# Performance work log

Measured on AMD Instinct MI355X. Metric: run time of the kernel, lower is better.

The kernel has to match this reference:

```python
import jax, jax.numpy as jnp
import numpy as np

N_NODES = 5000
N_EDGES = 80000
HIDDEN = 128
NUM_RBF = 64
MAX_Z = 128
CUTOFF_UPPER = 5.0
LN_EPS = 1e-5


def setup_inputs() -> dict:
    key = jax.random.key(0)
    ks = jax.random.split(key, 24)
    H, R = HIDDEN, NUM_RBF
    def lin(k, out_d, in_d):
        s = 1.0 / np.sqrt(in_d)
        return jax.random.uniform(k, (out_d, in_d), jnp.float32, -s, s)
    def bias(k, out_d, in_d):
        s = 1.0 / np.sqrt(in_d)
        return jax.random.uniform(k, (out_d,), jnp.float32, -s, s)
    v = jax.random.normal(ks[3], (N_EDGES, 3), jnp.float32)
    v = v / jnp.linalg.norm(v, axis=-1, keepdims=True)
    return {
        "z": jax.random.randint(ks[0], (N_NODES,), 0, MAX_Z),
        "edge_index": jax.random.randint(ks[1], (2, N_EDGES), 0, N_NODES),
        "edge_weight": jax.random.uniform(ks[2], (N_EDGES,), jnp.float32) * CUTOFF_UPPER * 0.9,
        "edge_vec_norm": v,
        "edge_attr": jax.random.normal(ks[4], (N_EDGES, R), jnp.float32),
        "emb": jax.random.normal(ks[5], (MAX_Z, H), jnp.float32),
        "W_emb2": lin(ks[6], H, 2 * H), "b_emb2": bias(ks[7], H, 2 * H),
        "Wd1": lin(ks[8], H, R), "bd1": bias(ks[9], H, R),
        "Wd2": lin(ks[10], H, R), "bd2": bias(ks[11], H, R),
        "Wd3": lin(ks[12], H, R), "bd3": bias(ks[13], H, R),
        "Wt1": lin(ks[14], H, H), "Wt2": lin(ks[15], H, H), "Wt3": lin(ks[16], H, H),
        "Ws1": lin(ks[17], 2 * H, H), "bs1": bias(ks[18], 2 * H, H),
        "Ws2": lin(ks[19], 3 * H, 2 * H), "bs2": bias(ks[20], 3 * H, 2 * H),
        "ln_g": jnp.ones((H,), jnp.float32),
        "ln_b": jnp.zeros((H,), jnp.float32),
    }


def _skew(v):
    # v: [E,3] -> [E,3,3] skew-symmetric
    z = jnp.zeros_like(v[:, 0])
    return jnp.stack(
        [z, -v[:, 2], v[:, 1], v[:, 2], z, -v[:, 0], -v[:, 1], v[:, 0], z], axis=1
    ).reshape(-1, 3, 3)


def _sym(v):
    # symmetric traceless part of outer product (outer product already symmetric)
    outer = v[:, :, None] * v[:, None, :]
    tr = jnp.trace(outer, axis1=-2, axis2=-1) / 3.0
    return outer - tr[:, None, None] * jnp.eye(3, dtype=v.dtype)


def reference(z, edge_index, edge_weight, edge_vec_norm, edge_attr,
              emb, W_emb2, b_emb2, Wd1, bd1, Wd2, bd2, Wd3, bd3,
              Wt1, Wt2, Wt3, Ws1, bs1, Ws2, bs2, ln_g, ln_b):
    N = z.shape[0]
    H = emb.shape[1]
    src, dst = edge_index[0], edge_index[1]

    # atomic number message Zij: [E,H]
    Z = emb[z]
    Zij = jnp.concatenate([Z[src], Z[dst]], axis=-1) @ W_emb2.T + b_emb2

    # cosine cutoff (cutoff_lower = 0)
    cut = 0.5 * (jnp.cos(edge_weight * (jnp.pi / CUTOFF_UPPER)) + 1.0)
    cut = cut * (edge_weight < CUTOFF_UPPER).astype(edge_weight.dtype)
    C = cut[:, None] * Zij  # [E,H]

    f1 = (edge_attr @ Wd1.T + bd1) * C  # [E,H]
    f2 = (edge_attr @ Wd2.T + bd2) * C
    f3 = (edge_attr @ Wd3.T + bd3) * C

    eye = jnp.eye(3, dtype=C.dtype)
    Iij = f1[:, :, None, None] * eye  # [E,H,3,3]
    Aij = f2[:, :, None, None] * _skew(edge_vec_norm)[:, None, :, :]
    Sij = f3[:, :, None, None] * _sym(edge_vec_norm)[:, None, :, :]

    I = jax.ops.segment_sum(Iij, src, num_segments=N)  # [N,H,3,3]
    A = jax.ops.segment_sum(Aij, src, num_segments=N)
    S = jax.ops.segment_sum(Sij, src, num_segments=N)

    # Frobenius norm per channel, LayerNorm, scalar MLP
    tn = ((I + A + S) ** 2).sum((-2, -1))  # [N,H]
    mu = tn.mean(-1, keepdims=True)
    var = tn.var(-1, keepdims=True)
    norm = (tn - mu) / jnp.sqrt(var + LN_EPS) * ln_g + ln_b
    norm = jax.nn.silu(norm @ Ws1.T + bs1)
    norm = jax.nn.silu(norm @ Ws2.T + bs2)
    norm = norm.reshape(N, H, 3)

    I = jnp.einsum('nhij,gh->ngij', I, Wt1) * norm[:, :, 0, None, None]
    A = jnp.einsum('nhij,gh->ngij', A, Wt2) * norm[:, :, 1, None, None]
    S = jnp.einsum('nhij,gh->ngij', S, Wt3) * norm[:, :, 2, None, None]
    return I + A + S
```

## Files before the change

### kernel.cpp

```cpp
#include <hip/hip_runtime.h>
#include <hip/hip_bf16.h>

#define NN   5000
#define NP   5008
#define NE   80000
#define HID  128
#define NRBF 64
#define PI_OVER_5 0.6283185307179586f
#define LN_EPS 1e-5f

typedef unsigned short bf16_t;
typedef __attribute__((ext_vector_type(8))) short short8;
typedef __attribute__((ext_vector_type(4))) float floatx4;

__device__ __forceinline__ bf16_t to_bf16(float x){
    union { float f; unsigned int u; } v; v.f = x;
    unsigned int r = v.u + 0x7fffu + ((v.u >> 16) & 1u);
    return (bf16_t)(r >> 16);
}
__device__ __forceinline__ float from_bf16(bf16_t h){
    union { unsigned int u; float f; } v; v.u = ((unsigned int)h) << 16;
    return v.f;
}
__device__ __forceinline__ uint4 pack8(const float* s){
    float4 a = *(const float4*)s;
    float4 b = *(const float4*)(s + 4);
    uint4 o;
    o.x = to_bf16(a.x) | ((unsigned)to_bf16(a.y) << 16);
    o.y = to_bf16(a.z) | ((unsigned)to_bf16(a.w) << 16);
    o.z = to_bf16(b.x) | ((unsigned)to_bf16(b.y) << 16);
    o.w = to_bf16(b.z) | ((unsigned)to_bf16(b.w) << 16);
    return o;
}

__global__ __launch_bounds__(128) void k_embtab(
    const float* __restrict__ W_emb2, const float* __restrict__ emb,
    float* __restrict__ embL, float* __restrict__ embR)
{
    int t = blockIdx.x;
    int h = threadIdx.x;
    const float* er = emb + t * HID;
    const float* wl = W_emb2 + (size_t)h * (2 * HID);
    float sl = 0.f, sr = 0.f;
    #pragma unroll 8
    for (int k = 0; k < HID; k++){
        float e = er[k];
        sl += wl[k] * e;
        sr += wl[HID + k] * e;
    }
    embL[t * HID + h] = sl;
    embR[t * HID + h] = sr;
}

__global__ __launch_bounds__(256) void k_prep_wts(
    const float* __restrict__ Wd1, const float* __restrict__ Wd2, const float* __restrict__ Wd3,
    const float* __restrict__ bd1, const float* __restrict__ bd2, const float* __restrict__ bd3,
    const float* __restrict__ Wt1, const float* __restrict__ Wt2, const float* __restrict__ Wt3,
    const float* __restrict__ Ws1, const float* __restrict__ Ws2,
    bf16_t* __restrict__ Wcat, bf16_t* __restrict__ Wtc,
    bf16_t* __restrict__ Ws1b, bf16_t* __restrict__ Ws2b, float* __restrict__ bdcat)
{
    int t = blockIdx.x * 256 + threadIdx.x;
    int i8 = t * 8;
    const float* src; bf16_t* dst;
    if (i8 < 24576){
        int j = i8; int tb = j >> 13; int r = j & 8191;
        src = ((tb == 0) ? Wd1 : (tb == 1) ? Wd2 : Wd3) + r; dst = Wcat + j;
    } else if (i8 < 24576 + 49152){
        int j = i8 - 24576; int tb = j >> 14; int r = j & 16383;
        src = ((tb == 0) ? Wt1 : (tb == 1) ? Wt2 : Wt3) + r; dst = Wtc + j;
    } else if (i8 < 24576 + 49152 + 32768){
        int j = i8 - 73728; src = Ws1 + j; dst = Ws1b + j;
    } else {
        int j = i8 - 106496; src = Ws2 + j; dst = Ws2b + j;
    }
    *(uint4*)dst = pack8(src);
    if (t < 384){
        int tb2 = t >> 7, ch2 = t & 127;
        const float* bsrc = (tb2 == 0) ? bd1 : ((tb2 == 1) ? bd2 : bd3);
        bdcat[t] = bsrc[ch2];
    }
}

__global__ void k_count(const int* __restrict__ ei, int* __restrict__ counts){
    int e = blockIdx.x * 256 + threadIdx.x;
    if (e < NE) atomicAdd(&counts[ei[e]], 1);
}

__global__ __launch_bounds__(1024) void k_scan(
    const int* __restrict__ counts, int* __restrict__ offsets, int* __restrict__ cursor)
{
    __shared__ int s[1024];
    const int t = threadIdx.x;
    const int CH = 5;
    int base = t * CH;
    int loc[CH];
    int lsum = 0;
    #pragma unroll
    for (int u = 0; u < CH; u++){
        int i = base + u;
        int v = (i < NN) ? counts[i] : 0;
        loc[u] = lsum;
        lsum += v;
    }
    s[t] = lsum;
    __syncthreads();
    for (int d = 1; d < 1024; d <<= 1){
        int v = (t >= d) ? s[t - d] : 0;
        __syncthreads();
        s[t] += v;
        __syncthreads();
    }
    int excl = s[t] - lsum;
    #pragma unroll
    for (int u = 0; u < CH; u++){
        int i = base + u;
        if (i < NN){ int o = excl + loc[u]; offsets[i] = o; cursor[i] = o; }
    }
    if (t == 1023) offsets[NN] = s[1023];
}

__global__ void k_fill(const int* __restrict__ ei, const int* __restrict__ z,
                       const float* __restrict__ ew, const float* __restrict__ evn,
                       int* __restrict__ cursor, int* __restrict__ elist,
                       float2* __restrict__ meta, float* __restrict__ evn_p){
    int e = blockIdx.x * 256 + threadIdx.x;
    if (e < NE){
        int sN = ei[e], dN = ei[NE + e];
        int p = atomicAdd(&cursor[sN], 1);
        elist[p] = e;
        float w = ew[e];
        float c = (w < 5.0f) ? 0.5f * (__cosf(w * PI_OVER_5) + 1.0f) : 0.0f;
        meta[p] = make_float2(c, __int_as_float(z[sN] | (z[dN] << 8)));
        evn_p[p*3+0] = evn[e*3+0];
        evn_p[p*3+1] = evn[e*3+1];
        evn_p[p*3+2] = evn[e*3+2];
    }
}

__global__ __launch_bounds__(256) void k_edge(
    const float* __restrict__ attr, const int* __restrict__ elist,
    const float2* __restrict__ meta,
    const bf16_t* __restrict__ Wcat, const float* __restrict__ bdcat,
    const float* __restrict__ embL, const float* __restrict__ embR,
    const float* __restrict__ b_emb2,
    bf16_t* __restrict__ f1, bf16_t* __restrict__ f2, bf16_t* __restrict__ f3)
{
    __shared__ __align__(16) bf16_t sB[64 * 72];
    __shared__ float sCut[64];
    __shared__ int   sZ[64];

    const int tid = threadIdx.x;
    const int p0  = blockIdx.x * 64;

    {
        int r = tid >> 2, qt = tid & 3;
        int e = elist[p0 + r];
        const float* ar = attr + (size_t)e * NRBF + qt * 16;
        uint4 o0 = pack8(ar);
        uint4 o1 = pack8(ar + 8);
        *(uint4*)&sB[r * 72 + qt * 16]     = o0;
        *(uint4*)&sB[r * 72 + qt * 16 + 8] = o1;
    }
    if (tid < 64){
        float2 m = meta[p0 + tid];
        sCut[tid] = m.x;
        sZ[tid]   = __float_as_int(m.y);
    }
    __syncthreads();

    const int wv = tid >> 6, lane = tid & 63;
    const int col = lane & 15, q = lane >> 4;

    floatx4 acc[6][4];
    #pragma unroll
    for (int mt = 0; mt < 6; mt++)
        #pragma unroll
        for (int nt = 0; nt < 4; nt++)
            acc[mt][nt] = (floatx4)(0.f);

    #pragma unroll
    for (int s = 0; s < 2; s++){
        short8 bf[4];
        #pragma unroll
        for (int nt = 0; nt < 4; nt++){
            int r = nt * 16 + col;
            bf[nt] = *(const short8*)&sB[r * 72 + s * 32 + q * 8];
        }
        short8 af[6];
        #pragma unroll
        for (int t = 0; t < 3; t++)
            #pragma unroll
            for (int c = 0; c < 2; c++){
                int m = t * 128 + wv * 32 + c * 16 + col;
                af[t * 2 + c] = *(const short8*)(Wcat + (size_t)m * NRBF + s * 32 + q * 8);
            }
        #pragma unroll
        for (int mt = 0; mt < 6; mt++)
            #pragma unroll
            for (int nt = 0; nt < 4; nt++)
                acc[mt][nt] = __builtin_amdgcn_mfma_f32_16x16x32_bf16(
                    af[mt], bf[nt], acc[mt][nt], 0, 0, 0);
    }

    floatx4 be[2], bd[3][2];
    #pragma unroll
    for (int c = 0; c < 2; c++){
        int ch4 = wv * 32 + c * 16 + q * 4;
        be[c] = *(const floatx4*)(b_emb2 + ch4);
        #pragma unroll
        for (int t = 0; t < 3; t++)
            bd[t][c] = *(const floatx4*)(bdcat + t * 128 + ch4);
    }
    bf16_t* const fs[3] = {f1, f2, f3};
    #pragma unroll
    for (int nt = 0; nt < 4; nt++){
        int e = nt * 16 + col;
        float cut = sCut[e];
        int zp = sZ[e];
        int zs = zp & 255, zd = zp >> 8;
        size_t orow = (size_t)(p0 + e) * HID;
        #pragma unroll
        for (int c = 0; c < 2; c++){
            int ch4 = wv * 32 + c * 16 + q * 4;
            floatx4 L = *(const floatx4*)(embL + zs * HID + ch4);
            floatx4 R = *(const floatx4*)(embR + zd * HID + ch4);
            floatx4 Cv = (L + R + be[c]) * cut;
            #pragma unroll
            for (int t = 0; t < 3; t++){
                floatx4 v = (acc[t * 2 + c][nt] + bd[t][c]) * Cv;
                uint2 pk;
                pk.x = to_bf16(v[0]) | ((unsigned)to_bf16(v[1]) << 16);
                pk.y = to_bf16(v[2]) | ((unsigned)to_bf16(v[3]) << 16);
                *(uint2*)(fs[t] + orow + ch4) = pk;
            }
        }
    }
}

__global__ __launch_bounds__(128) void k_gather(
    const int* __restrict__ offsets, const float* __restrict__ evn_p,
    const bf16_t* __restrict__ f1, const bf16_t* __restrict__ f2, const bf16_t* __restrict__ f3,
    const float* __restrict__ ln_g, const float* __restrict__ ln_b,
    bf16_t* __restrict__ acc, bf16_t* __restrict__ ln_out)
{
    const int n = blockIdx.x, h = threadIdx.x;
    const int s = offsets[n], e_end = offsets[n + 1];
    float c=0, ax=0, ay=0, az=0, sxx=0, syy=0, szz=0, sxy=0, sxz=0, syz=0;
    for (int idx = s; idx < e_end; idx++){
        float vx = evn_p[idx*3+0], vy = evn_p[idx*3+1], vz = evn_p[idx*3+2];
        float t3 = (vx*vx + vy*vy + vz*vz) * (1.f/3.f);
        float a = from_bf16(f1[(size_t)idx * HID + h]);
        float b = from_bf16(f2[(size_t)idx * HID + h]);
        float d = from_bf16(f3[(size_t)idx * HID + h]);
        c += a;
        ax += b * vx; ay += b * vy; az += b * vz;
        sxx += d * (vx*vx - t3); syy += d * (vy*vy - t3); szz += d * (vz*vz - t3);
        sxy += d * (vx*vy); sxz += d * (vx*vz); syz += d * (vy*vz);
    }
    const int PS = NP * HID;
    const int base = n * HID + h;
    acc[0*PS+base]=to_bf16(c);   acc[1*PS+base]=to_bf16(ax);
    acc[2*PS+base]=to_bf16(ay);  acc[3*PS+base]=to_bf16(az);
    acc[4*PS+base]=to_bf16(sxx); acc[5*PS+base]=to_bf16(syy);
    acc[6*PS+base]=to_bf16(szz); acc[7*PS+base]=to_bf16(sxy);
    acc[8*PS+base]=to_bf16(sxz); acc[9*PS+base]=to_bf16(syz);

    float tn = 3.f*c*c + 2.f*c*(sxx+syy+szz)
             + sxx*sxx + syy*syy + szz*szz
             + 2.f*(sxy*sxy + sxz*sxz + syz*syz)
             + 2.f*(ax*ax + ay*ay + az*az);

    __shared__ float r1[128], r2[128];
    r1[h] = tn; r2[h] = tn * tn;
    __syncthreads();
    for (int st = 64; st > 0; st >>= 1){
        if (h < st){ r1[h] += r1[h + st]; r2[h] += r2[h + st]; }
        __syncthreads();
    }
    float mu  = r1[0] * (1.f / HID);
    float var = r2[0] * (1.f / HID) - mu * mu;
    ln_out[base] = to_bf16((tn - mu) * rsqrtf(var + LN_EPS) * ln_g[h] + ln_b[h]);
}

__global__ __launch_bounds__(256) void k_node(
    const bf16_t* __restrict__ lnb, const bf16_t* __restrict__ accb,
    const bf16_t* __restrict__ Ws1b, const float* __restrict__ bs1,
    const bf16_t* __restrict__ Ws2b, const float* __restrict__ bs2,
    const bf16_t* __restrict__ Wtc,
    float* __restrict__ out)
{
    __shared__ __align__(16) bf16_t h1s[16 * 280];
    __shared__ float nrms[16 * 392];

    const int tid = threadIdx.x;
    const int wv = tid >> 6, lane = tid & 63;
    const int col = lane & 15, q = lane >> 4;
    const int n0 = blockIdx.x * 16;

    {
        short8 a1[4];
        #pragma unroll
        for (int k = 0; k < 4; k++)
            a1[k] = *(const short8*)(lnb + (size_t)(n0 + col) * HID + k * 32 + q * 8);
        floatx4 c1[4];
        #pragma unroll
        for (int nt = 0; nt < 4; nt++) c1[nt] = (floatx4)(0.f);
        #pragma unroll
        for (int nt = 0; nt < 4; nt++){
            int cg = wv * 64 + nt * 16 + col;
            #pragma unroll
            for (int k = 0; k < 4; k++){
                short8 b = *(const short8*)(Ws1b + (size_t)cg * HID + k * 32 + q * 8);
                c1[nt] = __builtin_amdgcn_mfma_f32_16x16x32_bf16(a1[k], b, c1[nt], 0, 0, 0);
            }
        }
        #pragma unroll
        for (int nt = 0; nt < 4; nt++){
            int cg = wv * 64 + nt * 16 + col;
            float bias = bs1[cg];
            #pragma unroll
            for (int r = 0; r < 4; r++){
                float v = c1[nt][r] + bias;
                v = v / (1.f + __expf(-v));
                h1s[(q * 4 + r) * 280 + cg] = to_bf16(v);
            }
        }
    }
    __syncthreads();

    {
        short8 a2[8];
        #pragma unroll
        for (int k = 0; k < 8; k++)
            a2[k] = *(const short8*)&h1s[col * 280 + k * 32 + q * 8];
        floatx4 c2[6];
        #pragma unroll
        for (int nt = 0; nt < 6; nt++) c2[nt] = (floatx4)(0.f);
        #pragma unroll
        for (int nt = 0; nt < 6; nt++){
            int cg = wv * 96 + nt * 16 + col;
            #pragma unroll
            for (int k = 0; k < 8; k++){
                short8 b = *(const short8*)(Ws2b + (size_t)cg * 256 + k * 32 + q * 8);
                c2[nt] = __builtin_amdgcn_mfma_f32_16x16x32_bf16(a2[k], b, c2[nt], 0, 0, 0);
            }
        }
        #pragma unroll
        for (int nt = 0; nt < 6; nt++){
            int cg = wv * 96 + nt * 16 + col;
            float bias = bs2[cg];
            #pragma unroll
            for (int r = 0; r < 4; r++){
                float v = c2[nt][r] + bias;
                v = v / (1.f + __expf(-v));
                nrms[(q * 4 + r) * 392 + cg] = v;
            }
        }
    }
    __syncthreads();

    floatx4 cm[10][2];
    #pragma unroll
    for (int p = 0; p < 10; p++){
        #pragma unroll
        for (int nt = 0; nt < 2; nt++) cm[p][nt] = (floatx4)(0.f);
    }
    #pragma unroll
    for (int p = 0; p < 10; p++){
        const bf16_t* ap = accb + (size_t)p * NP * HID + (size_t)(n0 + col) * HID;
        short8 a3[4];
        #pragma unroll
        for (int k = 0; k < 4; k++)
            a3[k] = *(const short8*)(ap + k * 32 + q * 8);
        int tb = (p == 0) ? 0 : ((p < 4) ? 1 : 2);
        #pragma unroll
        for (int nt = 0; nt < 2; nt++){
            int g = wv * 32 + nt * 16 + col;
            const bf16_t* wp = Wtc + tb * 16384 + (size_t)g * HID;
            #pragma unroll
            for (int k = 0; k < 4; k++){
                short8 b = *(const short8*)(wp + k * 32 + q * 8);
                cm[p][nt] = __builtin_amdgcn_mfma_f32_16x16x32_bf16(a3[k], b, cm[p][nt], 0, 0, 0);
            }
        }
    }
    #pragma unroll
    for (int nt = 0; nt < 2; nt++){
        int g = wv * 32 + nt * 16 + col;
        #pragma unroll
        for (int r = 0; r < 4; r++){
            int node = q * 4 + r;
            int n = n0 + node;
            if (n < NN){
                float n0f = nrms[node * 392 + g * 3 + 0];
                float n1f = nrms[node * 392 + g * 3 + 1];
                float n2f = nrms[node * 392 + g * 3 + 2];
                float c   = cm[0][nt][r];
                float ax  = cm[1][nt][r], ay = cm[2][nt][r], az = cm[3][nt][r];
                float sxx = cm[4][nt][r], syy= cm[5][nt][r], szz= cm[6][nt][r];
                float sxy = cm[7][nt][r], sxz= cm[8][nt][r], syz= cm[9][nt][r];
                float* o = out + ((size_t)n * HID + g) * 9;
                o[0] = n0f*c + n2f*sxx;   o[1] = n2f*sxy - n1f*az;  o[2] = n2f*sxz + n1f*ay;
                o[3] = n2f*sxy + n1f*az;  o[4] = n0f*c + n2f*syy;   o[5] = n2f*syz - n1f*ax;
                o[6] = n2f*sxz - n1f*ay;  o[7] = n2f*syz + n1f*ax;  o[8] = n0f*c + n2f*szz;
            }
        }
    }
}

extern "C" void kernel_launch(void* const* d_in, const int* in_sizes, int n_in,
                              void* d_out, int out_size, void* d_ws, size_t ws_size,
                              hipStream_t stream)
{
    (void)in_sizes; (void)n_in; (void)out_size; (void)ws_size;
    const int*   z      = (const int*)  d_in[0];
    const int*   ei     = (const int*)  d_in[1];
    const float* ew     = (const float*)d_in[2];
    const float* evn    = (const float*)d_in[3];
    const float* attr   = (const float*)d_in[4];
    const float* emb    = (const float*)d_in[5];
    const float* W_emb2 = (const float*)d_in[6];
    const float* b_emb2 = (const float*)d_in[7];
    const float* Wd1 = (const float*)d_in[8];  const float* bd1 = (const float*)d_in[9];
    const float* Wd2 = (const float*)d_in[10]; const float* bd2 = (const float*)d_in[11];
    const float* Wd3 = (const float*)d_in[12]; const float* bd3 = (const float*)d_in[13];
    const float* Wt1 = (const float*)d_in[14]; const float* Wt2 = (const float*)d_in[15];
    const float* Wt3 = (const float*)d_in[16];
    const float* Ws1 = (const float*)d_in[17]; const float* bs1 = (const float*)d_in[18];
    const float* Ws2 = (const float*)d_in[19]; const float* bs2 = (const float*)d_in[20];
    const float* ln_g = (const float*)d_in[21]; const float* ln_b = (const float*)d_in[22];
    float* out = (float*)d_out;

    char* ws = (char*)d_ws;
    size_t o = 0;
    auto take = [&](size_t b)->size_t{ size_t c = o; o += (b + 255) & ~(size_t)255; return c; };
    size_t f1_o  = take((size_t)NE * HID * 2);
    size_t f2_o  = take((size_t)NE * HID * 2);
    size_t f3_o  = take((size_t)NE * HID * 2);
    size_t acc_o = take((size_t)10 * NP * HID * 2);
    size_t ln_of = take((size_t)NP * HID * 2);
    size_t eL_o  = take((size_t)128 * HID * 4);
    size_t eR_o  = take((size_t)128 * HID * 4);
    size_t cnt_o = take((size_t)NN * 4);
    size_t off_o = take((size_t)(NN + 1) * 4);
    size_t cur_o = take((size_t)NN * 4);
    size_t el_o  = take((size_t)NE * 4);
    size_t met_o = take((size_t)NE * 8);
    size_t evp_o = take((size_t)NE * 12);
    size_t wc_o  = take((size_t)384 * 64 * 2);
    size_t wt_o  = take((size_t)3 * 128 * 128 * 2);
    size_t w1_o  = take((size_t)256 * 128 * 2);
    size_t w2_o  = take((size_t)384 * 256 * 2);
    size_t bdc_o = take((size_t)384 * 4);

    bf16_t* f1 = (bf16_t*)(ws + f1_o);
    bf16_t* f2 = (bf16_t*)(ws + f2_o);
    bf16_t* f3 = (bf16_t*)(ws + f3_o);
    bf16_t* accb = (bf16_t*)(ws + acc_o);
    bf16_t* lnb  = (bf16_t*)(ws + ln_of);
    float* embL = (float*)(ws + eL_o);
    float* embR = (float*)(ws + eR_o);
    int* counts = (int*)(ws + cnt_o);
    int* offs   = (int*)(ws + off_o);
    int* cursor = (int*)(ws + cur_o);
    int* elist  = (int*)(ws + el_o);
    float2* meta = (float2*)(ws + met_o);
    float* evn_p = (float*)(ws + evp_o);
    bf16_t* Wcat = (bf16_t*)(ws + wc_o);
    bf16_t* Wtc  = (bf16_t*)(ws + wt_o);
    bf16_t* Ws1b = (bf16_t*)(ws + w1_o);
    bf16_t* Ws2b = (bf16_t*)(ws + w2_o);
    float* bdcat = (float*)(ws + bdc_o);

    hipMemsetAsync(counts, 0, (size_t)NN * 4, stream);

    k_prep_wts<<<100, 256, 0, stream>>>(Wd1, Wd2, Wd3, bd1, bd2, bd3,
                                        Wt1, Wt2, Wt3, Ws1, Ws2,
                                        Wcat, Wtc, Ws1b, Ws2b, bdcat);
    k_embtab<<<128, 128, 0, stream>>>(W_emb2, emb, embL, embR);
    k_count <<<(NE + 255) / 256, 256, 0, stream>>>(ei, counts);
    k_scan  <<<1, 1024, 0, stream>>>(counts, offs, cursor);
    k_fill  <<<(NE + 255) / 256, 256, 0, stream>>>(ei, z, ew, evn, cursor, elist, meta, evn_p);
    k_edge  <<<NE / 64, 256, 0, stream>>>(attr, elist, meta, Wcat, bdcat,
                                          embL, embR, b_emb2, f1, f2, f3);
    k_gather<<<NN, 128, 0, stream>>>(offs, evn_p, f1, f2, f3, ln_g, ln_b, accb, lnb);
    k_node  <<<(NN + 15) / 16, 256, 0, stream>>>(lnb, accb, Ws1b, bs1, Ws2b, bs2, Wtc, out);
}
```

Baseline: 229.8 us.

## Fuse all stages into one persistent cooperative kernel with grid syncs

```diff
diff --git a/kernel.cpp b/kernel.cpp
--- a/kernel.cpp
+++ b/kernel.cpp
@@ -1,5 +1,8 @@
 #include <hip/hip_runtime.h>
 #include <hip/hip_bf16.h>
+#include <hip/hip_cooperative_groups.h>
+
+namespace cg = cooperative_groups;
 
 #define NN   5000
 #define NP   5008
@@ -33,379 +36,367 @@
     return o;
 }
 
-__global__ __launch_bounds__(128) void k_embtab(
-    const float* __restrict__ W_emb2, const float* __restrict__ emb,
-    float* __restrict__ embL, float* __restrict__ embR)
+struct KP {
+    const int *z, *ei;
+    const float *ew, *evn, *attr, *emb, *W_emb2, *b_emb2;
+    const float *Wd1, *bd1, *Wd2, *bd2, *Wd3, *bd3;
+    const float *Wt1, *Wt2, *Wt3, *Ws1, *bs1, *Ws2, *bs2, *ln_g, *ln_b;
+    bf16_t *Wcat, *Wtc, *Ws1b, *Ws2b;
+    float *bdcat, *embL, *embR;
+    int *counts, *offs, *cursor, *elist;
+    float2 *meta; float *evn_p;
+    bf16_t *f1, *f2, *f3, *accb, *lnb;
+    float *out;
+};
+
+struct ShEdge {
+    bf16_t sB[64 * 72];
+    float  sCut[64];
+    int    sZ[64];
+};
+struct ShScan { int s[256]; };
+struct ShGat  { float r1[4], r2[4]; };
+struct ShNode {
+    bf16_t h1s[16 * 280];
+    bf16_t nrms[16 * 392];
+};
+union ShAll { ShEdge edge; ShScan scan; ShGat gat; ShNode node; };
+
+__global__ __launch_bounds__(256, 2) void k_all(KP P)
 {
-    int t = blockIdx.x;
-    int h = threadIdx.x;
-    const float* er = emb + t * HID;
-    const float* wl = W_emb2 + (size_t)h * (2 * HID);
-    float sl = 0.f, sr = 0.f;
-    #pragma unroll 8
-    for (int k = 0; k < HID; k++){
-        float e = er[k];
-        sl += wl[k] * e;
-        sr += wl[HID + k] * e;
-    }
-    embL[t * HID + h] = sl;
-    embR[t * HID + h] = sr;
-}
-
-__global__ __launch_bounds__(256) void k_prep_wts(
-    const float* __restrict__ Wd1, const float* __restrict__ Wd2, const float* __restrict__ Wd3,
-    const float* __restrict__ bd1, const float* __restrict__ bd2, const float* __restrict__ bd3,
-    const float* __restrict__ Wt1, const float* __restrict__ Wt2, const float* __restrict__ Wt3,
-    const float* __restrict__ Ws1, const float* __restrict__ Ws2,
-    bf16_t* __restrict__ Wcat, bf16_t* __restrict__ Wtc,
-    bf16_t* __restrict__ Ws1b, bf16_t* __restrict__ Ws2b, float* __restrict__ bdcat)
-{
-    int t = blockIdx.x * 256 + threadIdx.x;
-    int i8 = t * 8;
-    const float* src; bf16_t* dst;
-    if (i8 < 24576){
-        int j = i8; int tb = j >> 13; int r = j & 8191;
-        src = ((tb == 0) ? Wd1 : (tb == 1) ? Wd2 : Wd3) + r; dst = Wcat + j;
-    } else if (i8 < 24576 + 49152){
-        int j = i8 - 24576; int tb = j >> 14; int r = j & 16383;
-        src = ((tb == 0) ? Wt1 : (tb == 1) ? Wt2 : Wt3) + r; dst = Wtc + j;
-    } else if (i8 < 24576 + 49152 + 32768){
-        int j = i8 - 73728; src = Ws1 + j; dst = Ws1b + j;
-    } else {
-        int j = i8 - 106496; src = Ws2 + j; dst = Ws2b + j;
-    }
-    *(uint4*)dst = pack8(src);
-    if (t < 384){
-        int tb2 = t >> 7, ch2 = t & 127;
-        const float* bsrc = (tb2 == 0) ? bd1 : ((tb2 == 1) ? bd2 : bd3);
-        bdcat[t] = bsrc[ch2];
-    }
-}
-
-__global__ void k_count(const int* __restrict__ ei, int* __restrict__ counts){
-    int e = blockIdx.x * 256 + threadIdx.x;
-    if (e < NE) atomicAdd(&counts[ei[e]], 1);
-}
-
-__global__ __launch_bounds__(1024) void k_scan(
-    const int* __restrict__ counts, int* __restrict__ offsets, int* __restrict__ cursor)
-{
-    __shared__ int s[1024];
-    const int t = threadIdx.x;
-    const int CH = 5;
-    int base = t * CH;
-    int loc[CH];
-    int lsum = 0;
-    #pragma unroll
-    for (int u = 0; u < CH; u++){
-        int i = base + u;
-        int v = (i < NN) ? counts[i] : 0;
-        loc[u] = lsum;
-        lsum += v;
-    }
-    s[t] = lsum;
-    __syncthreads();
-    for (int d = 1; d < 1024; d <<= 1){
-        int v = (t >= d) ? s[t - d] : 0;
-        __syncthreads();
-        s[t] += v;
-        __syncthreads();
-    }
-    int excl = s[t] - lsum;
-    #pragma unroll
-    for (int u = 0; u < CH; u++){
-        int i = base + u;
-        if (i < NN){ int o = excl + loc[u]; offsets[i] = o; cursor[i] = o; }
-    }
-    if (t == 1023) offsets[NN] = s[1023];
-}
-
-__global__ void k_fill(const int* __restrict__ ei, const int* __restrict__ z,
-                       const float* __restrict__ ew, const float* __restrict__ evn,
-                       int* __restrict__ cursor, int* __restrict__ elist,
-                       float2* __restrict__ meta, float* __restrict__ evn_p){
-    int e = blockIdx.x * 256 + threadIdx.x;
-    if (e < NE){
-        int sN = ei[e], dN = ei[NE + e];
-        int p = atomicAdd(&cursor[sN], 1);
-        elist[p] = e;
-        float w = ew[e];
-        float c = (w < 5.0f) ? 0.5f * (__cosf(w * PI_OVER_5) + 1.0f) : 0.0f;
-        meta[p] = make_float2(c, __int_as_float(z[sN] | (z[dN] << 8)));
-        evn_p[p*3+0] = evn[e*3+0];
-        evn_p[p*3+1] = evn[e*3+1];
-        evn_p[p*3+2] = evn[e*3+2];
-    }
-}
-
-__global__ __launch_bounds__(256) void k_edge(
-    const float* __restrict__ attr, const int* __restrict__ elist,
-    const float2* __restrict__ meta,
-    const bf16_t* __restrict__ Wcat, const float* __restrict__ bdcat,
-    const float* __restrict__ embL, const float* __restrict__ embR,
-    const float* __restrict__ b_emb2,
-    bf16_t* __restrict__ f1, bf16_t* __restrict__ f2, bf16_t* __restrict__ f3)
-{
-    __shared__ __align__(16) bf16_t sB[64 * 72];
-    __shared__ float sCut[64];
-    __shared__ int   sZ[64];
+    cg::grid_group grid = cg::this_grid();
+    __shared__ __align__(16) ShAll sh;
 
     const int tid = threadIdx.x;
-    const int p0  = blockIdx.x * 64;
-
-    {
-        int r = tid >> 2, qt = tid & 3;
-        int e = elist[p0 + r];
-        const float* ar = attr + (size_t)e * NRBF + qt * 16;
-        uint4 o0 = pack8(ar);
-        uint4 o1 = pack8(ar + 8);
-        *(uint4*)&sB[r * 72 + qt * 16]     = o0;
-        *(uint4*)&sB[r * 72 + qt * 16 + 8] = o1;
-    }
-    if (tid < 64){
-        float2 m = meta[p0 + tid];
-        sCut[tid] = m.x;
-        sZ[tid]   = __float_as_int(m.y);
-    }
-    __syncthreads();
-
+    const int bid = blockIdx.x;
+    const int nblk = gridDim.x;
+    const int gthreads = nblk * 256;
+    const int gt = bid * 256 + tid;
     const int wv = tid >> 6, lane = tid & 63;
     const int col = lane & 15, q = lane >> 4;
 
-    floatx4 acc[6][4];
-    #pragma unroll
-    for (int mt = 0; mt < 6; mt++)
-        #pragma unroll
-        for (int nt = 0; nt < 4; nt++)
-            acc[mt][nt] = (floatx4)(0.f);
-
-    #pragma unroll
-    for (int s = 0; s < 2; s++){
-        short8 bf[4];
-        #pragma unroll
-        for (int nt = 0; nt < 4; nt++){
-            int r = nt * 16 + col;
-            bf[nt] = *(const short8*)&sB[r * 72 + s * 32 + q * 8];
-        }
-        short8 af[6];
-        #pragma unroll
-        for (int t = 0; t < 3; t++)
-            #pragma unroll
-            for (int c = 0; c < 2; c++){
-                int m = t * 128 + wv * 32 + c * 16 + col;
-                af[t * 2 + c] = *(const short8*)(Wcat + (size_t)m * NRBF + s * 32 + q * 8);
-            }
+    for (int t = gt; t < 25600; t += gthreads){
+        int i8 = t * 8;
+        const float* src; bf16_t* dst;
+        if (i8 < 24576){
+            int j = i8; int tb = j >> 13; int r = j & 8191;
+            src = ((tb == 0) ? P.Wd1 : (tb == 1) ? P.Wd2 : P.Wd3) + r; dst = P.Wcat + j;
+        } else if (i8 < 24576 + 49152){
+            int j = i8 - 24576; int tb = j >> 14; int r = j & 16383;
+            src = ((tb == 0) ? P.Wt1 : (tb == 1) ? P.Wt2 : P.Wt3) + r; dst = P.Wtc + j;
+        } else if (i8 < 24576 + 49152 + 32768){
+            int j = i8 - 73728; src = P.Ws1 + j; dst = P.Ws1b + j;
+        } else {
+            int j = i8 - 106496; src = P.Ws2 + j; dst = P.Ws2b + j;
+        }
+        *(uint4*)dst = pack8(src);
+        if (t < 384){
+            int tb2 = t >> 7, ch2 = t & 127;
+            const float* bsrc = (tb2 == 0) ? P.bd1 : ((tb2 == 1) ? P.bd2 : P.bd3);
+            P.bdcat[t] = bsrc[ch2];
+        }
+    }
+    for (int t = gt; t < 32768; t += gthreads){
+        int type = t >> 8; int rest = t & 255;
+        int half = rest >> 7; int h = rest & 127;
+        const float* wl = P.W_emb2 + (size_t)h * (2 * HID) + half * HID;
+        const float* er = P.emb + type * HID;
+        float s = 0.f;
+        #pragma unroll 8
+        for (int k = 0; k < HID; k++) s += wl[k] * er[k];
+        (half ? P.embR : P.embL)[type * HID + h] = s;
+    }
+    for (int e = gt; e < NE; e += gthreads)
+        atomicAdd(&P.counts[P.ei[e]], 1);
+    grid.sync();
+
+    if (bid == 0){
+        const int CH = 20;
+        int base = tid * CH;
+        int loc[CH];
+        int lsum = 0;
+        #pragma unroll
+        for (int u = 0; u < CH; u++){
+            int i = base + u;
+            int v = (i < NN) ? P.counts[i] : 0;
+            loc[u] = lsum; lsum += v;
+        }
+        sh.scan.s[tid] = lsum;
+        __syncthreads();
+        for (int d = 1; d < 256; d <<= 1){
+            int v = (tid >= d) ? sh.scan.s[tid - d] : 0;
+            __syncthreads();
+            sh.scan.s[tid] += v;
+            __syncthreads();
+        }
+        int excl = sh.scan.s[tid] - lsum;
+        #pragma unroll
+        for (int u = 0; u < CH; u++){
+            int i = base + u;
+            if (i < NN){ int o = excl + loc[u]; P.offs[i] = o; P.cursor[i] = o; }
+        }
+        if (tid == 255) P.offs[NN] = sh.scan.s[255];
+    }
+    grid.sync();
+
+    for (int e = gt; e < NE; e += gthreads){
+        int sN = P.ei[e], dN = P.ei[NE + e];
+        int p = atomicAdd(&P.cursor[sN], 1);
+        P.elist[p] = e;
+        float w = P.ew[e];
+        float c = (w < 5.0f) ? 0.5f * (__cosf(w * PI_OVER_5) + 1.0f) : 0.0f;
+        P.meta[p] = make_float2(c, __int_as_float(P.z[sN] | (P.z[dN] << 8)));
+        P.evn_p[p*3+0] = P.evn[e*3+0];
+        P.evn_p[p*3+1] = P.evn[e*3+1];
+        P.evn_p[p*3+2] = P.evn[e*3+2];
+    }
+    grid.sync();
+
+    for (int tile = bid; tile < NE / 64; tile += nblk){
+        const int p0 = tile * 64;
+        __syncthreads();
+        {
+            int r = tid >> 2, qt = tid & 3;
+            int e = P.elist[p0 + r];
+            const float* ar = P.attr + (size_t)e * NRBF + qt * 16;
+            uint4 o0 = pack8(ar);
+            uint4 o1 = pack8(ar + 8);
+            *(uint4*)&sh.edge.sB[r * 72 + qt * 16]     = o0;
+            *(uint4*)&sh.edge.sB[r * 72 + qt * 16 + 8] = o1;
+        }
+        if (tid < 64){
+            float2 m = P.meta[p0 + tid];
+            sh.edge.sCut[tid] = m.x;
+            sh.edge.sZ[tid]   = __float_as_int(m.y);
+        }
+        __syncthreads();
+
+        floatx4 acc[6][4];
         #pragma unroll
         for (int mt = 0; mt < 6; mt++)
             #pragma unroll
             for (int nt = 0; nt < 4; nt++)
-                acc[mt][nt] = __builtin_amdgcn_mfma_f32_16x16x32_bf16(
-                    af[mt], bf[nt], acc[mt][nt], 0, 0, 0);
-    }
-
-    floatx4 be[2], bd[3][2];
-    #pragma unroll
-    for (int c = 0; c < 2; c++){
-        int ch4 = wv * 32 + c * 16 + q * 4;
-        be[c] = *(const floatx4*)(b_emb2 + ch4);
-        #pragma unroll
-        for (int t = 0; t < 3; t++)
-            bd[t][c] = *(const floatx4*)(bdcat + t * 128 + ch4);
-    }
-    bf16_t* const fs[3] = {f1, f2, f3};
-    #pragma unroll
-    for (int nt = 0; nt < 4; nt++){
-        int e = nt * 16 + col;
-        float cut = sCut[e];
-        int zp = sZ[e];
-        int zs = zp & 255, zd = zp >> 8;
-        size_t orow = (size_t)(p0 + e) * HID;
+                acc[mt][nt] = (floatx4)(0.f);
+
+        #pragma unroll
+        for (int s = 0; s < 2; s++){
+            short8 bf[4];
+            #pragma unroll
+            for (int nt = 0; nt < 4; nt++){
+                int r = nt * 16 + col;
+                bf[nt] = *(const short8*)&sh.edge.sB[r * 72 + s * 32 + q * 8];
+            }
+            short8 af[6];
+            #pragma unroll
+            for (int t = 0; t < 3; t++)
+                #pragma unroll
+                for (int c = 0; c < 2; c++){
+                    int m = t * 128 + wv * 32 + c * 16 + col;
+                    af[t * 2 + c] = *(const short8*)(P.Wcat + (size_t)m * NRBF + s * 32 + q * 8);
+                }
+            #pragma unroll
+            for (int mt = 0; mt < 6; mt++)
+                #pragma unroll
+                for (int nt = 0; nt < 4; nt++)
+                    acc[mt][nt] = __builtin_amdgcn_mfma_f32_16x16x32_bf16(
+                        af[mt], bf[nt], acc[mt][nt], 0, 0, 0);
+        }
+
+        floatx4 be[2], bd[3][2];
         #pragma unroll
         for (int c = 0; c < 2; c++){
             int ch4 = wv * 32 + c * 16 + q * 4;
-            floatx4 L = *(const floatx4*)(embL + zs * HID + ch4);
-            floatx4 R = *(const floatx4*)(embR + zd * HID + ch4);
-            floatx4 Cv = (L + R + be[c]) * cut;
-            #pragma unroll
-            for (int t = 0; t < 3; t++){
-                floatx4 v = (acc[t * 2 + c][nt] + bd[t][c]) * Cv;
-                uint2 pk;
-                pk.x = to_bf16(v[0]) | ((unsigned)to_bf16(v[1]) << 16);
-                pk.y = to_bf16(v[2]) | ((unsigned)to_bf16(v[3]) << 16);
-                *(uint2*)(fs[t] + orow + ch4) = pk;
-            }
-        }
-    }
-}
-
-__global__ __launch_bounds__(128) void k_gather(
-    const int* __restrict__ offsets, const float* __restrict__ evn_p,
-    const bf16_t* __restrict__ f1, const bf16_t* __restrict__ f2, const bf16_t* __restrict__ f3,
-    const float* __restrict__ ln_g, const float* __restrict__ ln_b,
-    bf16_t* __restrict__ acc, bf16_t* __restrict__ ln_out)
-{
-    const int n = blockIdx.x, h = threadIdx.x;
-    const int s = offsets[n], e_end = offsets[n + 1];
-    float c=0, ax=0, ay=0, az=0, sxx=0, syy=0, szz=0, sxy=0, sxz=0, syz=0;
-    for (int idx = s; idx < e_end; idx++){
-        float vx = evn_p[idx*3+0], vy = evn_p[idx*3+1], vz = evn_p[idx*3+2];
-        float t3 = (vx*vx + vy*vy + vz*vz) * (1.f/3.f);
-        float a = from_bf16(f1[(size_t)idx * HID + h]);
-        float b = from_bf16(f2[(size_t)idx * HID + h]);
-        float d = from_bf16(f3[(size_t)idx * HID + h]);
-        c += a;
-        ax += b * vx; ay += b * vy; az += b * vz;
-        sxx += d * (vx*vx - t3); syy += d * (vy*vy - t3); szz += d * (vz*vz - t3);
-        sxy += d * (vx*vy); sxz += d * (vx*vz); syz += d * (vy*vz);
-    }
-    const int PS = NP * HID;
-    const int base = n * HID + h;
-    acc[0*PS+base]=to_bf16(c);   acc[1*PS+base]=to_bf16(ax);
-    acc[2*PS+base]=to_bf16(ay);  acc[3*PS+base]=to_bf16(az);
-    acc[4*PS+base]=to_bf16(sxx); acc[5*PS+base]=to_bf16(syy);
-    acc[6*PS+base]=to_bf16(szz); acc[7*PS+base]=to_bf16(sxy);
-    acc[8*PS+base]=to_bf16(sxz); acc[9*PS+base]=to_bf16(syz);
-
-    float tn = 3.f*c*c + 2.f*c*(sxx+syy+szz)
-             + sxx*sxx + syy*syy + szz*szz
-             + 2.f*(sxy*sxy + sxz*sxz + syz*syz)
-             + 2.f*(ax*ax + ay*ay + az*az);
-
-    __shared__ float r1[128], r2[128];
-    r1[h] = tn; r2[h] = tn * tn;
-    __syncthreads();
-    for (int st = 64; st > 0; st >>= 1){
-        if (h < st){ r1[h] += r1[h + st]; r2[h] += r2[h + st]; }
-        __syncthreads();
-    }
-    float mu  = r1[0] * (1.f / HID);
-    float var = r2[0] * (1.f / HID) - mu * mu;
-    ln_out[base] = to_bf16((tn - mu) * rsqrtf(var + LN_EPS) * ln_g[h] + ln_b[h]);
-}
-
-__global__ __launch_bounds__(256) void k_node(
-    const bf16_t* __restrict__ lnb, const bf16_t* __restrict__ accb,
-    const bf16_t* __restrict__ Ws1b, const float* __restrict__ bs1,
-    const bf16_t* __restrict__ Ws2b, const float* __restrict__ bs2,
-    const bf16_t* __restrict__ Wtc,
-    float* __restrict__ out)
-{
-    __shared__ __align__(16) bf16_t h1s[16 * 280];
-    __shared__ float nrms[16 * 392];
-
-    const int tid = threadIdx.x;
-    const int wv = tid >> 6, lane = tid & 63;
-    const int col = lane & 15, q = lane >> 4;
-    const int n0 = blockIdx.x * 16;
+            be[c] = *(const floatx4*)(P.b_emb2 + ch4);
+            #pragma unroll
+            for (int t = 0; t < 3; t++)
+                bd[t][c] = *(const floatx4*)(P.bdcat + t * 128 + ch4);
+        }
+        bf16_t* const fs[3] = {P.f1, P.f2, P.f3};
+        #pragma unroll
+        for (int nt = 0; nt < 4; nt++){
+            int e = nt * 16 + col;
+            float cut = sh.edge.sCut[e];
+            int zp = sh.edge.sZ[e];
+            int zs = zp & 255, zd = zp >> 8;
+            size_t orow = (size_t)(p0 + e) * HID;
+            #pragma unroll
+            for (int c = 0; c < 2; c++){
+                int ch4 = wv * 32 + c * 16 + q * 4;
+                floatx4 L = *(const floatx4*)(P.embL + zs * HID + ch4);
+                floatx4 R = *(const floatx4*)(P.embR + zd * HID + ch4);
+                floatx4 Cv = (L + R + be[c]) * cut;
+                #pragma unroll
+                for (int t = 0; t < 3; t++){
+                    floatx4 v = (acc[t * 2 + c][nt] + bd[t][c]) * Cv;
+                    uint2 pk;
+                    pk.x = to_bf16(v[0]) | ((unsigned)to_bf16(v[1]) << 16);
+                    pk.y = to_bf16(v[2]) | ((unsigned)to_bf16(v[3]) << 16);
+                    *(uint2*)(fs[t] + orow + ch4) = pk;
+                }
+            }
+        }
+    }
+    grid.sync();
 
     {
-        short8 a1[4];
-        #pragma unroll
-        for (int k = 0; k < 4; k++)
-            a1[k] = *(const short8*)(lnb + (size_t)(n0 + col) * HID + k * 32 + q * 8);
-        floatx4 c1[4];
-        #pragma unroll
-        for (int nt = 0; nt < 4; nt++) c1[nt] = (floatx4)(0.f);
-        #pragma unroll
-        for (int nt = 0; nt < 4; nt++){
-            int cg = wv * 64 + nt * 16 + col;
-            #pragma unroll
-            for (int k = 0; k < 4; k++){
-                short8 b = *(const short8*)(Ws1b + (size_t)cg * HID + k * 32 + q * 8);
-                c1[nt] = __builtin_amdgcn_mfma_f32_16x16x32_bf16(a1[k], b, c1[nt], 0, 0, 0);
-            }
-        }
-        #pragma unroll
-        for (int nt = 0; nt < 4; nt++){
-            int cg = wv * 64 + nt * 16 + col;
-            float bias = bs1[cg];
+        const int half = tid >> 7, h = tid & 127;
+        for (int g = bid; g < NN / 2; g += nblk){
+            __syncthreads();
+            int n = g * 2 + half;
+            const int s = P.offs[n], e_end = P.offs[n + 1];
+            float c=0, ax=0, ay=0, az=0, sxx=0, syy=0, szz=0, sxy=0, sxz=0, syz=0;
+            for (int idx = s; idx < e_end; idx++){
+                float vx = P.evn_p[idx*3+0], vy = P.evn_p[idx*3+1], vz = P.evn_p[idx*3+2];
+                float t3 = (vx*vx + vy*vy + vz*vz) * (1.f/3.f);
+                float a = from_bf16(P.f1[(size_t)idx * HID + h]);
+                float b = from_bf16(P.f2[(size_t)idx * HID + h]);
+                float d = from_bf16(P.f3[(size_t)idx * HID + h]);
+                c += a;
+                ax += b * vx; ay += b * vy; az += b * vz;
+                sxx += d * (vx*vx - t3); syy += d * (vy*vy - t3); szz += d * (vz*vz - t3);
+                sxy += d * (vx*vy); sxz += d * (vx*vz); syz += d * (vy*vz);
+            }
+            float tn = 3.f*c*c + 2.f*c*(sxx+syy+szz)
+                     + sxx*sxx + syy*syy + szz*szz
+                     + 2.f*(sxy*sxy + sxz*sxz + syz*syz)
+                     + 2.f*(ax*ax + ay*ay + az*az);
+            float s1 = tn, s2 = tn * tn;
+            #pragma unroll
+            for (int d = 1; d < 64; d <<= 1){
+                s1 += __shfl_xor(s1, d);
+                s2 += __shfl_xor(s2, d);
+            }
+            if (lane == 0){ sh.gat.r1[wv] = s1; sh.gat.r2[wv] = s2; }
+            __syncthreads();
+            float mu  = (sh.gat.r1[half*2] + sh.gat.r1[half*2+1]) * (1.f / HID);
+            float var = (sh.gat.r2[half*2] + sh.gat.r2[half*2+1]) * (1.f / HID) - mu * mu;
+            float ln = (tn - mu) * rsqrtf(var + LN_EPS) * P.ln_g[h] + P.ln_b[h];
+            const size_t base = (size_t)n * HID + h;
+            P.lnb[base] = to_bf16(ln);
+            P.accb[(size_t)0 * NP * HID + base] = to_bf16(c);
+            P.accb[(size_t)1 * NP * HID + base] = to_bf16(ax);
+            P.accb[(size_t)2 * NP * HID + base] = to_bf16(ay);
+            P.accb[(size_t)3 * NP * HID + base] = to_bf16(az);
+            P.accb[(size_t)4 * NP * HID + base] = to_bf16(sxx);
+            P.accb[(size_t)5 * NP * HID + base] = to_bf16(syy);
+            P.accb[(size_t)6 * NP * HID + base] = to_bf16(szz);
+            P.accb[(size_t)7 * NP * HID + base] = to_bf16(sxy);
+            P.accb[(size_t)8 * NP * HID + base] = to_bf16(sxz);
+            P.accb[(size_t)9 * NP * HID + base] = to_bf16(syz);
+        }
+    }
+    grid.sync();
+
+    for (int g = bid; g < (NN + 15) / 16; g += nblk){
+        const int n0 = g * 16;
+        {
+            short8 a1[4];
+            #pragma unroll
+            for (int k = 0; k < 4; k++)
+                a1[k] = *(const short8*)(P.lnb + (size_t)(n0 + col) * HID + k * 32 + q * 8);
+            floatx4 c1[4];
+            #pragma unroll
+            for (int nt = 0; nt < 4; nt++) c1[nt] = (floatx4)(0.f);
+            #pragma unroll
+            for (int nt = 0; nt < 4; nt++){
+                int cg = wv * 64 + nt * 16 + col;
+                #pragma unroll
+                for (int k = 0; k < 4; k++){
+                    short8 b = *(const short8*)(P.Ws1b + (size_t)cg * HID + k * 32 + q * 8);
+                    c1[nt] = __builtin_amdgcn_mfma_f32_16x16x32_bf16(a1[k], b, c1[nt], 0, 0, 0);
+                }
+            }
+            #pragma unroll
+            for (int nt = 0; nt < 4; nt++){
+                int cg = wv * 64 + nt * 16 + col;
+                float bias = P.bs1[cg];
+                #pragma unroll
+                for (int r = 0; r < 4; r++){
+                    float v = c1[nt][r] + bias;
+                    v = v / (1.f + __expf(-v));
+                    sh.node.h1s[(q * 4 + r) * 280 + cg] = to_bf16(v);
+                }
+            }
+        }
+        __syncthreads();
+        {
+            short8 a2[8];
+            #pragma unroll
+            for (int k = 0; k < 8; k++)
+                a2[k] = *(const short8*)&sh.node.h1s[col * 280 + k * 32 + q * 8];
+            floatx4 c2[6];
+            #pragma unroll
+            for (int nt = 0; nt < 6; nt++) c2[nt] = (floatx4)(0.f);
+            #pragma unroll
+            for (int nt = 0; nt < 6; nt++){
+                int cg = wv * 96 + nt * 16 + col;
+                #pragma unroll
+                for (int k = 0; k < 8; k++){
+                    short8 b = *(const short8*)(P.Ws2b + (size_t)cg * 256 + k * 32 + q * 8);
+                    c2[nt] = __builtin_amdgcn_mfma_f32_16x16x32_bf16(a2[k], b, c2[nt], 0, 0, 0);
+                }
+            }
+            #pragma unroll
+            for (int nt = 0; nt < 6; nt++){
+                int cg = wv * 96 + nt * 16 + col;
+                float bias = P.bs2[cg];
+                #pragma unroll
+                for (int r = 0; r < 4; r++){
+                    float v = c2[nt][r] + bias;
+                    v = v / (1.f + __expf(-v));
+                    sh.node.nrms[(q * 4 + r) * 392 + cg] = to_bf16(v);
+                }
+            }
+        }
+        __syncthreads();
+        floatx4 cm[10][2];
+        #pragma unroll
+        for (int p = 0; p < 10; p++){
+            #pragma unroll
+            for (int nt = 0; nt < 2; nt++) cm[p][nt] = (floatx4)(0.f);
+        }
+        #pragma unroll
+        for (int p = 0; p < 10; p++){
+            const bf16_t* ap = P.accb + (size_t)p * NP * HID + (size_t)(n0 + col) * HID;
+            short8 a3[4];
+            #pragma unroll
+            for (int k = 0; k < 4; k++)
+                a3[k] = *(const short8*)(ap + k * 32 + q * 8);
+            int tb = (p == 0) ? 0 : ((p < 4) ? 1 : 2);
+            #pragma unroll
+            for (int nt = 0; nt < 2; nt++){
+                int gg = wv * 32 + nt * 16 + col;
+                const bf16_t* wp = P.Wtc + tb * 16384 + (size_t)gg * HID;
+                #pragma unroll
+                for (int k = 0; k < 4; k++){
+                    short8 b = *(const short8*)(wp + k * 32 + q * 8);
+                    cm[p][nt] = __builtin_amdgcn_mfma_f32_16x16x32_bf16(a3[k], b, cm[p][nt], 0, 0, 0);
+                }
+            }
+        }
+        #pragma unroll
+        for (int nt = 0; nt < 2; nt++){
+            int gg = wv * 32 + nt * 16 + col;
             #pragma unroll
             for (int r = 0; r < 4; r++){
-                float v = c1[nt][r] + bias;
-                v = v / (1.f + __expf(-v));
-                h1s[(q * 4 + r) * 280 + cg] = to_bf16(v);
-            }
-        }
-    }
-    __syncthreads();
-
-    {
-        short8 a2[8];
-        #pragma unroll
-        for (int k = 0; k < 8; k++)
-            a2[k] = *(const short8*)&h1s[col * 280 + k * 32 + q * 8];
-        floatx4 c2[6];
-        #pragma unroll
-        for (int nt = 0; nt < 6; nt++) c2[nt] = (floatx4)(0.f);
-        #pragma unroll
-        for (int nt = 0; nt < 6; nt++){
-            int cg = wv * 96 + nt * 16 + col;
-            #pragma unroll
-            for (int k = 0; k < 8; k++){
-                short8 b = *(const short8*)(Ws2b + (size_t)cg * 256 + k * 32 + q * 8);
-                c2[nt] = __builtin_amdgcn_mfma_f32_16x16x32_bf16(a2[k], b, c2[nt], 0, 0, 0);
-            }
-        }
-        #pragma unroll
-        for (int nt = 0; nt < 6; nt++){
-            int cg = wv * 96 + nt * 16 + col;
-            float bias = bs2[cg];
-            #pragma unroll
-            for (int r = 0; r < 4; r++){
-                float v = c2[nt][r] + bias;
-                v = v / (1.f + __expf(-v));
-                nrms[(q * 4 + r) * 392 + cg] = v;
-            }
-        }
-    }
-    __syncthreads();
-
-    floatx4 cm[10][2];
-    #pragma unroll
-    for (int p = 0; p < 10; p++){
-        #pragma unroll
-        for (int nt = 0; nt < 2; nt++) cm[p][nt] = (floatx4)(0.f);
-    }
-    #pragma unroll
-    for (int p = 0; p < 10; p++){
-        const bf16_t* ap = accb + (size_t)p * NP * HID + (size_t)(n0 + col) * HID;
-        short8 a3[4];
-        #pragma unroll
-        for (int k = 0; k < 4; k++)
-            a3[k] = *(const short8*)(ap + k * 32 + q * 8);
-        int tb = (p == 0) ? 0 : ((p < 4) ? 1 : 2);
-        #pragma unroll
-        for (int nt = 0; nt < 2; nt++){
-            int g = wv * 32 + nt * 16 + col;
-            const bf16_t* wp = Wtc + tb * 16384 + (size_t)g * HID;
-            #pragma unroll
-            for (int k = 0; k < 4; k++){
-                short8 b = *(const short8*)(wp + k * 32 + q * 8);
-                cm[p][nt] = __builtin_amdgcn_mfma_f32_16x16x32_bf16(a3[k], b, cm[p][nt], 0, 0, 0);
-            }
-        }
-    }
-    #pragma unroll
-    for (int nt = 0; nt < 2; nt++){
-        int g = wv * 32 + nt * 16 + col;
-        #pragma unroll
-        for (int r = 0; r < 4; r++){
-            int node = q * 4 + r;
-            int n = n0 + node;
-            if (n < NN){
-                float n0f = nrms[node * 392 + g * 3 + 0];
-                float n1f = nrms[node * 392 + g * 3 + 1];
-                float n2f = nrms[node * 392 + g * 3 + 2];
-                float c   = cm[0][nt][r];
-                float ax  = cm[1][nt][r], ay = cm[2][nt][r], az = cm[3][nt][r];
-                float sxx = cm[4][nt][r], syy= cm[5][nt][r], szz= cm[6][nt][r];
-                float sxy = cm[7][nt][r], sxz= cm[8][nt][r], syz= cm[9][nt][r];
-                float* o = out + ((size_t)n * HID + g) * 9;
-                o[0] = n0f*c + n2f*sxx;   o[1] = n2f*sxy - n1f*az;  o[2] = n2f*sxz + n1f*ay;
-                o[3] = n2f*sxy + n1f*az;  o[4] = n0f*c + n2f*syy;   o[5] = n2f*syz - n1f*ax;
-                o[6] = n2f*sxz - n1f*ay;  o[7] = n2f*syz + n1f*ax;  o[8] = n0f*c + n2f*szz;
-            }
-        }
+                int node = q * 4 + r;
+                int n = n0 + node;
+                if (n < NN){
+                    float n0f = from_bf16(sh.node.nrms[node * 392 + gg * 3 + 0]);
+                    float n1f = from_bf16(sh.node.nrms[node * 392 + gg * 3 + 1]);
+                    float n2f = from_bf16(sh.node.nrms[node * 392 + gg * 3 + 2]);
+                    float c   = cm[0][nt][r];
+                    float ax  = cm[1][nt][r], ay = cm[2][nt][r], az = cm[3][nt][r];
+                    float sxx = cm[4][nt][r], syy= cm[5][nt][r], szz= cm[6][nt][r];
+                    float sxy = cm[7][nt][r], sxz= cm[8][nt][r], syz= cm[9][nt][r];
+                    float* o = P.out + ((size_t)n * HID + gg) * 9;
+                    o[0] = n0f*c + n2f*sxx;   o[1] = n2f*sxy - n1f*az;  o[2] = n2f*sxz + n1f*ay;
+                    o[3] = n2f*sxy + n1f*az;  o[4] = n0f*c + n2f*syy;   o[5] = n2f*syz - n1f*ax;
+                    o[6] = n2f*sxz - n1f*ay;  o[7] = n2f*syz + n1f*ax;  o[8] = n0f*c + n2f*szz;
+                }
+            }
+        }
+        __syncthreads();
     }
 }
 
@@ -414,23 +405,24 @@
                               hipStream_t stream)
 {
     (void)in_sizes; (void)n_in; (void)out_size; (void)ws_size;
-    const int*   z      = (const int*)  d_in[0];
-    const int*   ei     = (const int*)  d_in[1];
-    const float* ew     = (const float*)d_in[2];
-    const float* evn    = (const float*)d_in[3];
-    const float* attr   = (const float*)d_in[4];
-    const float* emb    = (const float*)d_in[5];
-    const float* W_emb2 = (const float*)d_in[6];
-    const float* b_emb2 = (const float*)d_in[7];
-    const float* Wd1 = (const float*)d_in[8];  const float* bd1 = (const float*)d_in[9];
-    const float* Wd2 = (const float*)d_in[10]; const float* bd2 = (const float*)d_in[11];
-    const float* Wd3 = (const float*)d_in[12]; const float* bd3 = (const float*)d_in[13];
-    const float* Wt1 = (const float*)d_in[14]; const float* Wt2 = (const float*)d_in[15];
-    const float* Wt3 = (const float*)d_in[16];
-    const float* Ws1 = (const float*)d_in[17]; const float* bs1 = (const float*)d_in[18];
-    const float* Ws2 = (const float*)d_in[19]; const float* bs2 = (const float*)d_in[20];
-    const float* ln_g = (const float*)d_in[21]; const float* ln_b = (const float*)d_in[22];
-    float* out = (float*)d_out;
+    KP kp;
+    kp.z      = (const int*)  d_in[0];
+    kp.ei     = (const int*)  d_in[1];
+    kp.ew     = (const float*)d_in[2];
+    kp.evn    = (const float*)d_in[3];
+    kp.attr   = (const float*)d_in[4];
+    kp.emb    = (const float*)d_in[5];
+    kp.W_emb2 = (const float*)d_in[6];
+    kp.b_emb2 = (const float*)d_in[7];
+    kp.Wd1 = (const float*)d_in[8];  kp.bd1 = (const float*)d_in[9];
+    kp.Wd2 = (const float*)d_in[10]; kp.bd2 = (const float*)d_in[11];
+    kp.Wd3 = (const float*)d_in[12]; kp.bd3 = (const float*)d_in[13];
+    kp.Wt1 = (const float*)d_in[14]; kp.Wt2 = (const float*)d_in[15];
+    kp.Wt3 = (const float*)d_in[16];
+    kp.Ws1 = (const float*)d_in[17]; kp.bs1 = (const float*)d_in[18];
+    kp.Ws2 = (const float*)d_in[19]; kp.bs2 = (const float*)d_in[20];
+    kp.ln_g = (const float*)d_in[21]; kp.ln_b = (const float*)d_in[22];
+    kp.out = (float*)d_out;
 
     char* ws = (char*)d_ws;
     size_t o = 0;
@@ -454,36 +446,34 @@
     size_t w2_o  = take((size_t)384 * 256 * 2);
     size_t bdc_o = take((size_t)384 * 4);
 
-    bf16_t* f1 = (bf16_t*)(ws + f1_o);
-    bf16_t* f2 = (bf16_t*)(ws + f2_o);
-    bf16_t* f3 = (bf16_t*)(ws + f3_o);
-    bf16_t* accb = (bf16_t*)(ws + acc_o);
-    bf16_t* lnb  = (bf16_t*)(ws + ln_of);
-    float* embL = (float*)(ws + eL_o);
-    float* embR = (float*)(ws + eR_o);
-    int* counts = (int*)(ws + cnt_o);
-    int* offs   = (int*)(ws + off_o);
-    int* cursor = (int*)(ws + cur_o);
-    int* elist  = (int*)(ws + el_o);
-    float2* meta = (float2*)(ws + met_o);
-    float* evn_p = (float*)(ws + evp_o);
-    bf16_t* Wcat = (bf16_t*)(ws + wc_o);
-    bf16_t* Wtc  = (bf16_t*)(ws + wt_o);
-    bf16_t* Ws1b = (bf16_t*)(ws + w1_o);
-    bf16_t* Ws2b = (bf16_t*)(ws + w2_o);
-    float* bdcat = (float*)(ws + bdc_o);
-
-    hipMemsetAsync(counts, 0, (size_t)NN * 4, stream);
-
-    k_prep_wts<<<100, 256, 0, stream>>>(Wd1, Wd2, Wd3, bd1, bd2, bd3,
-                                        Wt1, Wt2, Wt3, Ws1, Ws2,
-                                        Wcat, Wtc, Ws1b, Ws2b, bdcat);
-    k_embtab<<<128, 128, 0, stream>>>(W_emb2, emb, embL, embR);
-    k_count <<<(NE + 255) / 256, 256, 0, stream>>>(ei, counts);
-    k_scan  <<<1, 1024, 0, stream>>>(counts, offs, cursor);
-    k_fill  <<<(NE + 255) / 256, 256, 0, stream>>>(ei, z, ew, evn, cursor, elist, meta, evn_p);
-    k_edge  <<<NE / 64, 256, 0, stream>>>(attr, elist, meta, Wcat, bdcat,
-                                          embL, embR, b_emb2, f1, f2, f3);
-    k_gather<<<NN, 128, 0, stream>>>(offs, evn_p, f1, f2, f3, ln_g, ln_b, accb, lnb);
-    k_node  <<<(NN + 15) / 16, 256, 0, stream>>>(lnb, accb, Ws1b, bs1, Ws2b, bs2, Wtc, out);
+    kp.f1 = (bf16_t*)(ws + f1_o);
+    kp.f2 = (bf16_t*)(ws + f2_o);
+    kp.f3 = (bf16_t*)(ws + f3_o);
+    kp.accb = (bf16_t*)(ws + acc_o);
+    kp.lnb  = (bf16_t*)(ws + ln_of);
+    kp.embL = (float*)(ws + eL_o);
+    kp.embR = (float*)(ws + eR_o);
+    kp.counts = (int*)(ws + cnt_o);
+    kp.offs   = (int*)(ws + off_o);
+    kp.cursor = (int*)(ws + cur_o);
+    kp.elist  = (int*)(ws + el_o);
+    kp.meta   = (float2*)(ws + met_o);
+    kp.evn_p  = (float*)(ws + evp_o);
+    kp.Wcat = (bf16_t*)(ws + wc_o);
+    kp.Wtc  = (bf16_t*)(ws + wt_o);
+    kp.Ws1b = (bf16_t*)(ws + w1_o);
+    kp.Ws2b = (bf16_t*)(ws + w2_o);
+    kp.bdcat = (float*)(ws + bdc_o);
+
+    hipMemsetAsync(kp.counts, 0, (size_t)NN * 4, stream);
+
+    int maxb = 0;
+    if (hipOccupancyMaxActiveBlocksPerMultiprocessor(
+            &maxb, (const void*)k_all, 256, 0) != hipSuccess || maxb < 1)
+        maxb = 1;
+    int grid = maxb * 256;
+    if (grid > 1024) grid = 1024;
+
+    void* args[] = { (void*)&kp };
+    hipLaunchCooperativeKernel((const void*)k_all, dim3(grid), dim3(256), args, 0, stream);
 }
```

After: 479.8 us. 109% more time.
